# Kernel tuning notes

Hardware: AMD Instinct MI355X
Metric: run time of the kernel (lower is better)

The kernel has to match this reference:

```python
import jax, jax.numpy as jnp
import numpy as np
from functools import partial

D_MODEL, D_STATE, D_CONV, EXPAND = 1024, 16, 4, 2
D_INNER = D_MODEL * EXPAND
B_SZ, L = 4, 2048


def setup_inputs() -> dict:
    key = jax.random.key(0)
    ks = jax.random.split(key, 8)
    s = 0.02
    A_init = jnp.log(jnp.arange(1, D_STATE + 1, dtype=jnp.float32))
    return {
        "x": jax.random.normal(ks[0], (B_SZ, L, D_MODEL), jnp.float32),
        "norm_w": jnp.ones((D_MODEL,), jnp.float32),
        "norm_b": jnp.zeros((D_MODEL,), jnp.float32),
        "W_in": jax.random.normal(ks[1], (D_MODEL, 2 * D_INNER), jnp.float32) * s,
        "conv_w": jax.random.normal(ks[2], (D_INNER, 1, D_CONV), jnp.float32) * 0.3,
        "conv_b": jnp.zeros((D_INNER,), jnp.float32),
        "A_log": jnp.broadcast_to(A_init, (D_INNER, D_STATE)).copy(),
        "W_b": jax.random.normal(ks[3], (D_INNER, D_STATE), jnp.float32) * s,
        "W_c": jax.random.normal(ks[4], (D_INNER, D_STATE), jnp.float32) * s,
        "W_delta": jax.random.normal(ks[5], (D_INNER, D_INNER), jnp.float32) * s,
        "b_delta": jnp.zeros((D_INNER,), jnp.float32),
        "D_param": jnp.ones((D_INNER,), jnp.float32),
        "W_out": jax.random.normal(ks[6], (D_INNER, D_MODEL), jnp.float32) * s,
    }


def _layernorm(x, w, b, eps=1e-5):
    mu = jnp.mean(x, axis=-1, keepdims=True)
    var = jnp.mean(jnp.square(x - mu), axis=-1, keepdims=True)
    return (x - mu) * jax.lax.rsqrt(var + eps) * w + b


def reference(x, norm_w, norm_b, W_in, conv_w, conv_b, A_log, W_b, W_c,
              W_delta, b_delta, D_param, W_out):
    residual = x
    xn = _layernorm(x, norm_w, norm_b)
    xz = jnp.einsum('bld,de->ble', xn, W_in)  # [B, L, 2*D_inner]
    x_path, z = jnp.split(xz, 2, axis=-1)

    # depthwise causal conv1d (torch pads both sides K-1 then slices [:L] == left-pad K-1)
    xc = jnp.moveaxis(x_path, 1, 2)  # [B, D_inner, L]
    xc = jax.lax.conv_general_dilated(
        xc, conv_w, window_strides=(1,), padding=[(D_CONV - 1, 0)],
        dimension_numbers=('NCH', 'OIH', 'NCH'), feature_group_count=D_INNER)
    xc = xc + conv_b[None, :, None]
    x_path = jax.nn.silu(jnp.moveaxis(xc, 2, 1))  # [B, L, D_inner]

    Bm = jnp.einsum('bld,dn->bln', x_path, W_b)   # [B, L, N]
    Cm = jnp.einsum('bld,dn->bln', x_path, W_c)   # [B, L, N]
    delta = jax.nn.softplus(jnp.einsum('bld,de->ble', x_path, W_delta) + b_delta)
    A = -jnp.exp(A_log)  # [D_inner, N]

    def step(h, inp):
        xt, dt, Bt, Ct = inp  # xt,dt: [B,D]; Bt,Ct: [B,N]
        A_bar = jnp.exp(dt[..., None] * A)              # [B, D, N]
        h = A_bar * h + (dt * xt)[..., None] * Bt[:, None, :]
        y = jnp.einsum('bdn,bn->bd', h, Ct) + D_param * xt
        return h, y

    h0 = jnp.zeros((x.shape[0], D_INNER, D_STATE), x_path.dtype)
    xs = (jnp.moveaxis(x_path, 1, 0), jnp.moveaxis(delta, 1, 0),
          jnp.moveaxis(Bm, 1, 0), jnp.moveaxis(Cm, 1, 0))
    _, ys = jax.lax.scan(step, h0, xs)           # ys: [L, B, D_inner]
    y = jnp.moveaxis(ys, 0, 1)                   # [B, L, D_inner]

    return jnp.einsum('bld,de->ble', y * jax.nn.silu(z), W_out) + residual
```

## Files before the change

### kernel.cpp

```cpp
#include <hip/hip_runtime.h>
#include <hip/hip_bf16.h>

#define D_MODEL 1024
#define D_STATE 16
#define D_INNER 2048
#define BSZ     4
#define SEQ     2048
#define NTOK    (BSZ*SEQ)
#define NBIG    2176
#define NCH     16
#define TC      128

typedef __attribute__((ext_vector_type(8))) short short8;
typedef __attribute__((ext_vector_type(4))) float floatx4;

__device__ __forceinline__ ushort bf2us(float f)
{
    union { __hip_bfloat16 h; ushort u; } c;
    c.h = __float2bfloat16(f);
    return c.u;
}
__device__ __forceinline__ float us2f(ushort u)
{
    union { uint u; float f; } c;
    c.u = ((uint)u) << 16;
    return c.f;
}
__device__ __forceinline__ uint pk2(float a, float b)
{
    return (uint)bf2us(a) | ((uint)bf2us(b) << 16);
}
__device__ __forceinline__ float blo(uint u) { return __uint_as_float(u << 16); }
__device__ __forceinline__ float bhi(uint u) { return __uint_as_float(u & 0xffff0000u); }
__device__ __forceinline__ float softplus_f(float v)
{
    return (v > 20.f) ? v : __logf(1.f + __expf(v));
}

__device__ __forceinline__ void load_lds16(const __hip_bfloat16* g, __hip_bfloat16* l)
{
    __builtin_amdgcn_global_load_lds(
        (const __attribute__((address_space(1))) char*)g,
        (__attribute__((address_space(3))) char*)l, 16, 0, 0);
}

__global__ __launch_bounds__(256) void ln_kernel(
    const float* __restrict__ x, const float* __restrict__ w,
    const float* __restrict__ bvec, __hip_bfloat16* __restrict__ out)
{
    int token = blockIdx.x;
    int tid = threadIdx.x;
    const float4 v = ((const float4*)(x + (size_t)token * D_MODEL))[tid];
    float s  = v.x + v.y + v.z + v.w;
    float sq = v.x*v.x + v.y*v.y + v.z*v.z + v.w*v.w;
#pragma unroll
    for (int o = 32; o; o >>= 1) { s += __shfl_down(s, o, 64); sq += __shfl_down(sq, o, 64); }
    __shared__ float red[8];
    int wid = tid >> 6;
    if ((tid & 63) == 0) { red[wid] = s; red[wid + 4] = sq; }
    __syncthreads();
    s  = red[0] + red[1] + red[2] + red[3];
    sq = red[4] + red[5] + red[6] + red[7];
    float mu  = s * (1.f / D_MODEL);
    float var = sq * (1.f / D_MODEL) - mu * mu;
    float rs  = rsqrtf(var + 1e-5f);
    float4 wv = ((const float4*)w)[tid];
    float4 bv = ((const float4*)bvec)[tid];
    union { ushort4 u; __hip_bfloat16 h[4]; } p;
    p.h[0] = __float2bfloat16((v.x - mu) * rs * wv.x + bv.x);
    p.h[1] = __float2bfloat16((v.y - mu) * rs * wv.y + bv.y);
    p.h[2] = __float2bfloat16((v.z - mu) * rs * wv.z + bv.z);
    p.h[3] = __float2bfloat16((v.w - mu) * rs * wv.w + bv.w);
    ((ushort4*)(out + (size_t)token * D_MODEL))[tid] = p.u;
}

__device__ __forceinline__ void tr_body(
    const float* __restrict__ src, __hip_bfloat16* __restrict__ dst,
    int R, int C, int dstStride, int dstRowOff, int bx, int by, int tx, int ty)
{
    __shared__ float tile[32][33];
#pragma unroll
    for (int i = 0; i < 4; ++i) {
        int r = by * 32 + ty + i * 8;
        int c = bx * 32 + tx;
        if (r < R && c < C) tile[ty + i * 8][tx] = src[(size_t)r * C + c];
    }
    __syncthreads();
#pragma unroll
    for (int i = 0; i < 4; ++i) {
        int c = bx * 32 + ty + i * 8;
        int r = by * 32 + tx;
        if (c < C && r < R)
            dst[(size_t)(dstRowOff + c) * dstStride + r] = __float2bfloat16(tile[tx][ty + i * 8]);
    }
}

__global__ __launch_bounds__(256) void transpose_cast(
    const float* __restrict__ src, __hip_bfloat16* __restrict__ dst,
    int R, int C, int dstStride, int dstRowOff)
{
    tr_body(src, dst, R, C, dstStride, dstRowOff,
            blockIdx.x, blockIdx.y, threadIdx.x, threadIdx.y);
}

__global__ __launch_bounds__(256) void prep_w(
    const float* __restrict__ W_in, const float* __restrict__ W_delta,
    const float* __restrict__ W_b, const float* __restrict__ W_c,
    __hip_bfloat16* __restrict__ wT1, __hip_bfloat16* __restrict__ wT2)
{
    int s = blockIdx.x;
    int tx = threadIdx.x, ty = threadIdx.y;
    if (s < 4096) {
        tr_body(W_in, wT1, 1024, 4096, 1024, 0, s & 127, s >> 7, tx, ty);
    } else if (s < 8192) {
        int q = s - 4096;
        tr_body(W_delta, wT2, 2048, 2048, 2048, 0, q & 63, q >> 6, tx, ty);
    } else if (s < 8256) {
        tr_body(W_b, wT2, 2048, 16, 2048, 2048, 0, s - 8192, tx, ty);
    } else if (s < 8320) {
        tr_body(W_c, wT2, 2048, 16, 2048, 2064, 0, s - 8256, tx, ty);
    } else {
        int i = (s - 8320) * 256 + ty * 32 + tx;
        uint4 z = {0, 0, 0, 0};
        ((uint4*)(wT2 + (size_t)2080 * 2048))[i] = z;
    }
}

template <int MODE>
__device__ __forceinline__ void gemm_body(
    const __hip_bfloat16* __restrict__ A, const __hip_bfloat16* __restrict__ BT,
    int M, int N, int K,
    float* __restrict__ outF,
    __hip_bfloat16* __restrict__ outB1, __hip_bfloat16* __restrict__ outB2,
    const float* __restrict__ extra)
{
    __shared__ __align__(16) __hip_bfloat16 As[128 * 64];
    __shared__ __align__(16) __hip_bfloat16 Bs[128 * 64];
    int tid = threadIdx.x;
    int m0 = blockIdx.x * 128;
    int n0 = blockIdx.y * 128;
    int wv = tid >> 6, lane = tid & 63;
    int wm = (wv >> 1) * 64, wn = (wv & 1) * 64;
    int lr = lane & 15, lq = lane >> 4;

    int srow = wv * 8 + (lane >> 3);
    int scg  = (lane & 7) ^ (lane >> 3);
    const __hip_bfloat16* Ag = A  + (size_t)(m0 + srow) * K + scg * 8;
    const __hip_bfloat16* Bg = BT + (size_t)(n0 + srow) * K + scg * 8;
    __hip_bfloat16* AsW = As + (wv * 8) * 64;
    __hip_bfloat16* BsW = Bs + (wv * 8) * 64;

    int swz = lq ^ (lr & 7);

    floatx4 acc[4][4] = {};

    for (int k0 = 0; k0 < K; k0 += 64) {
        __syncthreads();
#pragma unroll
        for (int i = 0; i < 4; ++i) {
            load_lds16(Ag + (size_t)(i * 32) * K + k0, AsW + i * 32 * 64);
            load_lds16(Bg + (size_t)(i * 32) * K + k0, BsW + i * 32 * 64);
        }
        __syncthreads();
#pragma unroll
        for (int kk = 0; kk < 2; ++kk) {
            int cofs = (swz ^ (kk << 2)) * 8;
            short8 af[4], bf[4];
#pragma unroll
            for (int mi = 0; mi < 4; ++mi)
                af[mi] = *(const short8*)(As + (wm + mi * 16 + lr) * 64 + cofs);
#pragma unroll
            for (int ni = 0; ni < 4; ++ni)
                bf[ni] = *(const short8*)(Bs + (wn + ni * 16 + lr) * 64 + cofs);
#pragma unroll
            for (int mi = 0; mi < 4; ++mi)
#pragma unroll
                for (int ni = 0; ni < 4; ++ni)
                    acc[mi][ni] = __builtin_amdgcn_mfma_f32_16x16x32_bf16(af[mi], bf[ni], acc[mi][ni], 0, 0, 0);
        }
    }

#pragma unroll
    for (int mi = 0; mi < 4; ++mi)
#pragma unroll
        for (int ni = 0; ni < 4; ++ni)
#pragma unroll
            for (int r = 0; r < 4; ++r) {
                int rg = m0 + wm + mi * 16 + lq * 4 + r;
                int cg = n0 + wn + ni * 16 + lr;
                float v = acc[mi][ni][r];
                if (MODE == 1) {
                    if (cg < D_INNER) {
                        outB1[(size_t)rg * D_INNER + cg] = __float2bfloat16(v);
                    } else {
                        float sv = v / (1.f + __expf(-v));
                        outB2[(size_t)rg * D_INNER + (cg - D_INNER)] = __float2bfloat16(sv);
                    }
                } else if (MODE == 2) {
                    if (cg < D_INNER) {
                        outB1[(size_t)rg * D_INNER + cg] = __float2bfloat16(softplus_f(v + extra[cg]));
                    } else if (cg < D_INNER + 32) {
                        outB2[(size_t)rg * 32 + (cg - D_INNER)] = __float2bfloat16(v);
                    }
                } else {
                    outF[(size_t)rg * D_MODEL + cg] = v + extra[(size_t)rg * D_MODEL + cg];
                }
            }
}

__global__ __launch_bounds__(256) void gemm_xz(
    const __hip_bfloat16* __restrict__ A, const __hip_bfloat16* __restrict__ BT,
    int M, int N, int K, float* __restrict__ outF,
    __hip_bfloat16* __restrict__ o1, __hip_bfloat16* __restrict__ o2,
    const float* __restrict__ extra)
{ gemm_body<1>(A, BT, M, N, K, outF, o1, o2, extra); }

__global__ __launch_bounds__(256) void gemm_dbc(
    const __hip_bfloat16* __restrict__ A, const __hip_bfloat16* __restrict__ BT,
    int M, int N, int K, float* __restrict__ outF,
    __hip_bfloat16* __restrict__ o1, __hip_bfloat16* __restrict__ o2,
    const float* __restrict__ extra)
{ gemm_body<2>(A, BT, M, N, K, outF, o1, o2, extra); }

__global__ __launch_bounds__(256) void gemm_out(
    const __hip_bfloat16* __restrict__ A, const __hip_bfloat16* __restrict__ BT,
    int M, int N, int K, float* __restrict__ outF,
    __hip_bfloat16* __restrict__ o1, __hip_bfloat16* __restrict__ o2,
    const float* __restrict__ extra)
{ gemm_body<3>(A, BT, M, N, K, outF, o1, o2, extra); }

__global__ __launch_bounds__(256) void conv_silu(
    const __hip_bfloat16* __restrict__ xin, const float* __restrict__ cw,
    const float* __restrict__ cb, __hip_bfloat16* __restrict__ xp)
{
    int gid = blockIdx.x * 256 + threadIdx.x;
    int d = gid & (D_INNER - 1);
    int rest = gid >> 11;
    int b = rest & 3;
    int ch = rest >> 2;
    int t0 = ch * 64;
    float w0 = cw[d * 4 + 0], w1 = cw[d * 4 + 1], w2 = cw[d * 4 + 2], w3 = cw[d * 4 + 3];
    float bias = cb[d];
    const __hip_bfloat16* base = xin + (size_t)b * SEQ * D_INNER + d;
    __hip_bfloat16* ob = xp + (size_t)b * SEQ * D_INNER + d;
    float xm3 = (t0 >= 3) ? __bfloat162float(base[(size_t)(t0 - 3) * D_INNER]) : 0.f;
    float xm2 = (t0 >= 2) ? __bfloat162float(base[(size_t)(t0 - 2) * D_INNER]) : 0.f;
    float xm1 = (t0 >= 1) ? __bfloat162float(base[(size_t)(t0 - 1) * D_INNER]) : 0.f;
#pragma unroll 4
    for (int t = t0; t < t0 + 64; ++t) {
        float xcur = __bfloat162float(base[(size_t)t * D_INNER]);
        float v = bias + w0 * xm3 + w1 * xm2 + w2 * xm1 + w3 * xcur;
        float sv = v / (1.f + __expf(-v));
        ob[(size_t)t * D_INNER] = __float2bfloat16(sv);
        xm3 = xm2; xm2 = xm1; xm1 = xcur;
    }
}


#define LOAD_A16() \
    const float4* Ar = (const float4*)(A_log + (size_t)d * D_STATE); \
    float4 aA = Ar[0], aB = Ar[1], aC = Ar[2], aD = Ar[3]; \
    float A0 = -__expf(aA.x), A1 = -__expf(aA.y), A2 = -__expf(aA.z), A3 = -__expf(aA.w); \
    float A4 = -__expf(aB.x), A5 = -__expf(aB.y), A6 = -__expf(aB.z), A7 = -__expf(aB.w); \
    float A8 = -__expf(aC.x), A9 = -__expf(aC.y), A10 = -__expf(aC.z), A11 = -__expf(aC.w); \
    float A12 = -__expf(aD.x), A13 = -__expf(aD.y), A14 = -__expf(aD.z), A15 = -__expf(aD.w)

#define UNPACK16(P, r0, r1) \
    float P##0 = blo(r0.x), P##1 = bhi(r0.x), P##2 = blo(r0.y), P##3 = bhi(r0.y); \
    float P##4 = blo(r0.z), P##5 = bhi(r0.z), P##6 = blo(r0.w), P##7 = bhi(r0.w); \
    float P##8 = blo(r1.x), P##9 = bhi(r1.x), P##10 = blo(r1.y), P##11 = bhi(r1.y); \
    float P##12 = blo(r1.z), P##13 = bhi(r1.z), P##14 = blo(r1.w), P##15 = bhi(r1.w)

#define SCAN_STEP_B() do { \
    float dtx = dt * xt; \
    h0  = __expf(dt * A0)  * h0  + dtx * B0; \
    h1  = __expf(dt * A1)  * h1  + dtx * B1; \
    h2  = __expf(dt * A2)  * h2  + dtx * B2; \
    h3  = __expf(dt * A3)  * h3  + dtx * B3; \
    h4  = __expf(dt * A4)  * h4  + dtx * B4; \
    h5  = __expf(dt * A5)  * h5  + dtx * B5; \
    h6  = __expf(dt * A6)  * h6  + dtx * B6; \
    h7  = __expf(dt * A7)  * h7  + dtx * B7; \
    h8  = __expf(dt * A8)  * h8  + dtx * B8; \
    h9  = __expf(dt * A9)  * h9  + dtx * B9; \
    h10 = __expf(dt * A10) * h10 + dtx * B10; \
    h11 = __expf(dt * A11) * h11 + dtx * B11; \
    h12 = __expf(dt * A12) * h12 + dtx * B12; \
    h13 = __expf(dt * A13) * h13 + dtx * B13; \
    h14 = __expf(dt * A14) * h14 + dtx * B14; \
    h15 = __expf(dt * A15) * h15 + dtx * B15; \
} while (0)

__global__ __launch_bounds__(256) void scan_p1(
    const ushort* __restrict__ dtb, const ushort* __restrict__ xpb,
    const ushort* __restrict__ BC, const float* __restrict__ A_log,
    ushort* __restrict__ hloc, ushort* __restrict__ prod)
{
    int gid = blockIdx.x * 256 + threadIdx.x;
    int d  = gid & (D_INNER - 1);
    int ch = (gid >> 11) & (NCH - 1);
    int b  = gid >> 15;
    LOAD_A16();
    float h0 = 0.f, h1 = 0.f, h2 = 0.f, h3 = 0.f, h4 = 0.f, h5 = 0.f, h6 = 0.f, h7 = 0.f;
    float h8 = 0.f, h9 = 0.f, h10 = 0.f, h11 = 0.f, h12 = 0.f, h13 = 0.f, h14 = 0.f, h15 = 0.f;
    float dtsum = 0.f;
    size_t mBase = (size_t)b * SEQ + (size_t)ch * TC;
    const ushort* dtp = dtb + mBase * D_INNER + d;
    const ushort* xpp = xpb + mBase * D_INNER + d;
    const uint4*  bcp = (const uint4*)(BC + mBase * 32);
    float dt = us2f(dtp[0]);
    float xt = us2f(xpp[0]);
    uint4 r0 = bcp[0], r1 = bcp[1];
    for (int t = 0; t < TC - 1; ++t) {
        float dt_n = us2f(dtp[(size_t)(t + 1) * D_INNER]);
        float xt_n = us2f(xpp[(size_t)(t + 1) * D_INNER]);
        uint4 r0_n = bcp[(t + 1) * 4 + 0];
        uint4 r1_n = bcp[(t + 1) * 4 + 1];
        {
            UNPACK16(B, r0, r1);
            dtsum += dt;
            SCAN_STEP_B();
        }
        dt = dt_n; xt = xt_n; r0 = r0_n; r1 = r1_n;
    }
    {
        UNPACK16(B, r0, r1);
        dtsum += dt;
        SCAN_STEP_B();
    }
    size_t idx = ((size_t)(b * NCH + ch) * D_INNER + d) * D_STATE;
    uint4 ho, h2v, po, p2v;
    ho.x  = pk2(h0, h1);   ho.y  = pk2(h2, h3);
    ho.z  = pk2(h4, h5);   ho.w  = pk2(h6, h7);
    h2v.x = pk2(h8, h9);   h2v.y = pk2(h10, h11);
    h2v.z = pk2(h12, h13); h2v.w = pk2(h14, h15);
    po.x  = pk2(__expf(dtsum * A0),  __expf(dtsum * A1));
    po.y  = pk2(__expf(dtsum * A2),  __expf(dtsum * A3));
    po.z  = pk2(__expf(dtsum * A4),  __expf(dtsum * A5));
    po.w  = pk2(__expf(dtsum * A6),  __expf(dtsum * A7));
    p2v.x = pk2(__expf(dtsum * A8),  __expf(dtsum * A9));
    p2v.y = pk2(__expf(dtsum * A10), __expf(dtsum * A11));
    p2v.z = pk2(__expf(dtsum * A12), __expf(dtsum * A13));
    p2v.w = pk2(__expf(dtsum * A14), __expf(dtsum * A15));
    ((uint4*)(hloc + idx))[0] = ho; ((uint4*)(hloc + idx))[1] = h2v;
    ((uint4*)(prod + idx))[0] = po; ((uint4*)(prod + idx))[1] = p2v;
}

__global__ __launch_bounds__(256) void scan_p2(
    const ushort* __restrict__ dtb, const ushort* __restrict__ xpb,
    const ushort* __restrict__ BC, const float* __restrict__ A_log,
    const float* __restrict__ D_param, const ushort* __restrict__ hloc,
    const ushort* __restrict__ prod, ushort* __restrict__ zio)
{
    int gid = blockIdx.x * 256 + threadIdx.x;
    int d  = gid & (D_INNER - 1);
    int ch = (gid >> 11) & (NCH - 1);
    int b  = gid >> 15;
    LOAD_A16();
    float Dp = D_param[d];
    float h0 = 0.f, h1 = 0.f, h2 = 0.f, h3 = 0.f, h4 = 0.f, h5 = 0.f, h6 = 0.f, h7 = 0.f;
    float h8 = 0.f, h9 = 0.f, h10 = 0.f, h11 = 0.f, h12 = 0.f, h13 = 0.f, h14 = 0.f, h15 = 0.f;
    for (int j = 0; j < ch; ++j) {
        size_t jdx = ((size_t)(b * NCH + j) * D_INNER + d) * D_STATE;
        uint4 a0 = ((const uint4*)(hloc + jdx))[0];
        uint4 a1 = ((const uint4*)(hloc + jdx))[1];
        uint4 q0 = ((const uint4*)(prod + jdx))[0];
        uint4 q1 = ((const uint4*)(prod + jdx))[1];
        h0  = blo(a0.x) + blo(q0.x) * h0;   h1  = bhi(a0.x) + bhi(q0.x) * h1;
        h2  = blo(a0.y) + blo(q0.y) * h2;   h3  = bhi(a0.y) + bhi(q0.y) * h3;
        h4  = blo(a0.z) + blo(q0.z) * h4;   h5  = bhi(a0.z) + bhi(q0.z) * h5;
        h6  = blo(a0.w) + blo(q0.w) * h6;   h7  = bhi(a0.w) + bhi(q0.w) * h7;
        h8  = blo(a1.x) + blo(q1.x) * h8;   h9  = bhi(a1.x) + bhi(q1.x) * h9;
        h10 = blo(a1.y) + blo(q1.y) * h10;  h11 = bhi(a1.y) + bhi(q1.y) * h11;
        h12 = blo(a1.z) + blo(q1.z) * h12;  h13 = bhi(a1.z) + bhi(q1.z) * h13;
        h14 = blo(a1.w) + blo(q1.w) * h14;  h15 = bhi(a1.w) + bhi(q1.w) * h15;
    }
    size_t mBase = (size_t)b * SEQ + (size_t)ch * TC;
    const ushort* dtp = dtb + mBase * D_INNER + d;
    const ushort* xpp = xpb + mBase * D_INNER + d;
    const uint4*  bcp = (const uint4*)(BC + mBase * 32);
    ushort* zp = zio + mBase * D_INNER + d;
    float dt = us2f(dtp[0]);
    float xt = us2f(xpp[0]);
    uint4 r0 = bcp[0], r1 = bcp[1], r2 = bcp[2], r3 = bcp[3];
    for (int t = 0; t < TC; ++t) {
        float dt_n = 0.f, xt_n = 0.f;
        uint4 r0_n = {0,0,0,0}, r1_n = {0,0,0,0}, r2_n = {0,0,0,0}, r3_n = {0,0,0,0};
        if (t < TC - 1) {
            dt_n = us2f(dtp[(size_t)(t + 1) * D_INNER]);
            xt_n = us2f(xpp[(size_t)(t + 1) * D_INNER]);
            r0_n = bcp[(t + 1) * 4 + 0];
            r1_n = bcp[(t + 1) * 4 + 1];
            r2_n = bcp[(t + 1) * 4 + 2];
            r3_n = bcp[(t + 1) * 4 + 3];
        }
        {
            UNPACK16(B, r0, r1);
            UNPACK16(C, r2, r3);
            float dtx = dt * xt;
            float y = Dp * xt;
            h0  = __expf(dt * A0)  * h0  + dtx * B0;   y += h0  * C0;
            h1  = __expf(dt * A1)  * h1  + dtx * B1;   y += h1  * C1;
            h2  = __expf(dt * A2)  * h2  + dtx * B2;   y += h2  * C2;
            h3  = __expf(dt * A3)  * h3  + dtx * B3;   y += h3  * C3;
            h4  = __expf(dt * A4)  * h4  + dtx * B4;   y += h4  * C4;
            h5  = __expf(dt * A5)  * h5  + dtx * B5;   y += h5  * C5;
            h6  = __expf(dt * A6)  * h6  + dtx * B6;   y += h6  * C6;
            h7  = __expf(dt * A7)  * h7  + dtx * B7;   y += h7  * C7;
            h8  = __expf(dt * A8)  * h8  + dtx * B8;   y += h8  * C8;
            h9  = __expf(dt * A9)  * h9  + dtx * B9;   y += h9  * C9;
            h10 = __expf(dt * A10) * h10 + dtx * B10;  y += h10 * C10;
            h11 = __expf(dt * A11) * h11 + dtx * B11;  y += h11 * C11;
            h12 = __expf(dt * A12) * h12 + dtx * B12;  y += h12 * C12;
            h13 = __expf(dt * A13) * h13 + dtx * B13;  y += h13 * C13;
            h14 = __expf(dt * A14) * h14 + dtx * B14;  y += h14 * C14;
            h15 = __expf(dt * A15) * h15 + dtx * B15;  y += h15 * C15;
            float z = us2f(zp[(size_t)t * D_INNER]);
            zp[(size_t)t * D_INNER] = bf2us(y * z);
        }
        dt = dt_n; xt = xt_n; r0 = r0_n; r1 = r1_n; r2 = r2_n; r3 = r3_n;
    }
}

extern "C" void kernel_launch(void* const* d_in, const int* in_sizes, int n_in,
                              void* d_out, int out_size, void* d_ws, size_t ws_size,
                              hipStream_t stream)
{
    const float* x       = (const float*)d_in[0];
    const float* norm_w  = (const float*)d_in[1];
    const float* norm_b  = (const float*)d_in[2];
    const float* W_in    = (const float*)d_in[3];
    const float* conv_w  = (const float*)d_in[4];
    const float* conv_b  = (const float*)d_in[5];
    const float* A_log   = (const float*)d_in[6];
    const float* W_b     = (const float*)d_in[7];
    const float* W_c     = (const float*)d_in[8];
    const float* W_delta = (const float*)d_in[9];
    const float* b_delta = (const float*)d_in[10];
    const float* D_param = (const float*)d_in[11];
    const float* W_out   = (const float*)d_in[12];
    float* out = (float*)d_out;

    char* ws = (char*)d_ws;
    char* R1 = ws;
    char* R2 = R1 + (size_t)33554432;
    char* R3 = R2 + (size_t)33554432;
    char* R4 = R3 + (size_t)33554432;
    char* R5 = R4 + (size_t)8912896;

    __hip_bfloat16* xnb  = (__hip_bfloat16*)R1;
    __hip_bfloat16* wT1  = (__hip_bfloat16*)(R1 + 16777216);
    __hip_bfloat16* xp   = (__hip_bfloat16*)R1;
    __hip_bfloat16* xraw = (__hip_bfloat16*)R2;
    __hip_bfloat16* dtb  = (__hip_bfloat16*)R2;
    __hip_bfloat16* wT3  = (__hip_bfloat16*)R2;
    __hip_bfloat16* zio  = (__hip_bfloat16*)R3;
    __hip_bfloat16* wT2  = (__hip_bfloat16*)R4;
    ushort*         hloc = (ushort*)R4;
    ushort*         prodb= (ushort*)(R4 + 4194304);
    __hip_bfloat16* BCb  = (__hip_bfloat16*)R5;

    ln_kernel<<<NTOK, 256, 0, stream>>>(x, norm_w, norm_b, xnb);

    prep_w<<<8416, dim3(32, 8), 0, stream>>>(W_in, W_delta, W_b, W_c, wT1, wT2);

    gemm_xz<<<dim3(NTOK / 128, 4096 / 128), 256, 0, stream>>>(
        xnb, wT1, NTOK, 4096, 1024, nullptr, xraw, zio, nullptr);

    conv_silu<<<1024, 256, 0, stream>>>(xraw, conv_w, conv_b, xp);

    gemm_dbc<<<dim3(NTOK / 128, NBIG / 128), 256, 0, stream>>>(
        xp, wT2, NTOK, NBIG, 2048, nullptr, dtb, BCb, b_delta);

    scan_p1<<<512, 256, 0, stream>>>((const ushort*)dtb, (const ushort*)xp,
                                     (const ushort*)BCb, A_log, hloc, prodb);
    scan_p2<<<512, 256, 0, stream>>>((const ushort*)dtb, (const ushort*)xp,
                                     (const ushort*)BCb, A_log, D_param,
                                     hloc, prodb, (ushort*)zio);

    transpose_cast<<<dim3(32, 64), dim3(32, 8), 0, stream>>>(W_out, wT3, 2048, 1024, 2048, 0);

    gemm_out<<<dim3(NTOK / 128, D_MODEL / 128), 256, 0, stream>>>(
        zio, wT3, NTOK, D_MODEL, 2048, out, nullptr, nullptr, x);

    (void)in_sizes; (void)n_in; (void)out_size; (void)ws_size;
}
```

Baseline: 568.8 us.

## Use 256x256 double-buffered GEMM for in-proj and delta, split-K B/C GEMM

Replaces the 128x128 GEMMs for the input projection and the delta projection with a new 256x256-tile, 512-thread kernel. It double-buffers LDS, prefetches the next K tile during MFMA phases, and raises wave priority around the MFMA blocks. The small B/C projection is moved out of the padded delta GEMM into a dedicated split-K kernel that writes fp32 partials, followed by a reduction kernel that converts them to bf16. The aim is more data reuse per tile and no wasted padded columns, at the cost of 128KB of LDS per block, lower occupancy, and an extra launch plus a scratch buffer for the partials.

```diff
diff --git a/kernel.cpp b/kernel.cpp
--- a/kernel.cpp
+++ b/kernel.cpp
@@ -7,7 +7,6 @@
 #define BSZ     4
 #define SEQ     2048
 #define NTOK    (BSZ*SEQ)
-#define NBIG    2176
 #define NCH     16
 #define TC      128
 
@@ -126,6 +125,124 @@
     }
 }
 
+
+#define G256_STG_A(kt_, pb_) do { \
+    const __hip_bfloat16* s_ = Ag + (size_t)(kt_) * 64; \
+    __hip_bfloat16* d_ = &As[pb_][wv * 512]; \
+    load_lds16(s_,                   d_); \
+    load_lds16(s_ + (size_t)64 * K,  d_ + 4096); \
+    load_lds16(s_ + (size_t)128 * K, d_ + 8192); \
+    load_lds16(s_ + (size_t)192 * K, d_ + 12288); \
+} while (0)
+
+#define G256_STG_B(kt_, pb_) do { \
+    const __hip_bfloat16* s_ = Bg + (size_t)(kt_) * 64; \
+    __hip_bfloat16* d_ = &Bs[pb_][wv * 512]; \
+    load_lds16(s_,                   d_); \
+    load_lds16(s_ + (size_t)64 * K,  d_ + 4096); \
+    load_lds16(s_ + (size_t)128 * K, d_ + 8192); \
+    load_lds16(s_ + (size_t)192 * K, d_ + 12288); \
+} while (0)
+
+#define G256_PHASE(mih_, nih_, ...) do { \
+    short8 af_[4][2], bf_[2][2]; \
+    _Pragma("unroll") \
+    for (int mi4 = 0; mi4 < 4; ++mi4) \
+      _Pragma("unroll") \
+      for (int kk = 0; kk < 2; ++kk) \
+        af_[mi4][kk] = *(const short8*)&As[p][((wm * 128 + ((mih_)*4 + mi4) * 16 + lr) << 6) \
+                                             + ((lq ^ (kk << 2) ^ (lr & 7)) << 3)]; \
+    _Pragma("unroll") \
+    for (int ni2 = 0; ni2 < 2; ++ni2) \
+      _Pragma("unroll") \
+      for (int kk = 0; kk < 2; ++kk) \
+        bf_[ni2][kk] = *(const short8*)&Bs[p][((wn * 64 + ((nih_)*2 + ni2) * 16 + lr) << 6) \
+                                             + ((lq ^ (kk << 2) ^ (lr & 7)) << 3)]; \
+    __VA_ARGS__; \
+    __builtin_amdgcn_s_barrier(); \
+    __builtin_amdgcn_s_setprio(1); \
+    _Pragma("unroll") \
+    for (int kk = 0; kk < 2; ++kk) \
+      _Pragma("unroll") \
+      for (int mi4 = 0; mi4 < 4; ++mi4) \
+        _Pragma("unroll") \
+        for (int ni2 = 0; ni2 < 2; ++ni2) \
+          acc[(mih_)*4 + mi4][(nih_)*2 + ni2] = __builtin_amdgcn_mfma_f32_16x16x32_bf16( \
+              af_[mi4][kk], bf_[ni2][kk], acc[(mih_)*4 + mi4][(nih_)*2 + ni2], 0, 0, 0); \
+    __builtin_amdgcn_s_setprio(0); \
+    __builtin_amdgcn_s_barrier(); \
+} while (0)
+
+template <int MODE, int K>
+__device__ __forceinline__ void gemm256_body(
+    const __hip_bfloat16* __restrict__ A, const __hip_bfloat16* __restrict__ BT,
+    __hip_bfloat16* __restrict__ out1, __hip_bfloat16* __restrict__ out2,
+    const float* __restrict__ extra)
+{
+    __shared__ __align__(16) __hip_bfloat16 As[2][256 * 64];
+    __shared__ __align__(16) __hip_bfloat16 Bs[2][256 * 64];
+    const int tid = threadIdx.x;
+    const int wv = tid >> 6, lane = tid & 63;
+    const int wm = wv >> 2, wn = wv & 3;
+    const int lr = lane & 15, lq = lane >> 4;
+    const int m0 = blockIdx.x * 256, n0 = blockIdx.y * 256;
+    const int srow8 = lane >> 3;
+    const int scg = (lane & 7) ^ srow8;
+    const __hip_bfloat16* Ag = A  + (size_t)(m0 + wv * 8 + srow8) * K + scg * 8;
+    const __hip_bfloat16* Bg = BT + (size_t)(n0 + wv * 8 + srow8) * K + scg * 8;
+
+    floatx4 acc[8][4] = {};
+    constexpr int NT = K / 64;
+
+    G256_STG_A(0, 0);
+    G256_STG_B(0, 0);
+    asm volatile("s_waitcnt vmcnt(0)" ::: "memory");
+    __builtin_amdgcn_s_barrier();
+
+#pragma unroll 2
+    for (int kt = 0; kt < NT; ++kt) {
+        const int p = kt & 1;
+        const bool pf = (kt + 1 < NT);
+        G256_PHASE(0, 0, if (pf) G256_STG_A(kt + 1, p ^ 1));
+        G256_PHASE(0, 1, if (pf) G256_STG_B(kt + 1, p ^ 1));
+        G256_PHASE(1, 0, (void)0);
+        G256_PHASE(1, 1, (void)0);
+        asm volatile("s_waitcnt vmcnt(0)" ::: "memory");
+        __builtin_amdgcn_s_barrier();
+    }
+
+#pragma unroll
+    for (int mi = 0; mi < 8; ++mi)
+#pragma unroll
+        for (int ni = 0; ni < 4; ++ni)
+#pragma unroll
+            for (int r = 0; r < 4; ++r) {
+                int rg = m0 + wm * 128 + mi * 16 + lq * 4 + r;
+                int cg = n0 + wn * 64 + ni * 16 + lr;
+                float v = acc[mi][ni][r];
+                if (MODE == 1) {
+                    if (cg < D_INNER) {
+                        out1[(size_t)rg * D_INNER + cg] = __float2bfloat16(v);
+                    } else {
+                        float sv = v / (1.f + __expf(-v));
+                        out2[(size_t)rg * D_INNER + (cg - D_INNER)] = __float2bfloat16(sv);
+                    }
+                } else {
+                    out1[(size_t)rg * D_INNER + cg] = __float2bfloat16(softplus_f(v + extra[cg]));
+                }
+            }
+}
+
+__global__ __launch_bounds__(512, 2) void gemm256_xz(
+    const __hip_bfloat16* __restrict__ A, const __hip_bfloat16* __restrict__ BT,
+    __hip_bfloat16* __restrict__ o1, __hip_bfloat16* __restrict__ o2)
+{ gemm256_body<1, 1024>(A, BT, o1, o2, nullptr); }
+
+__global__ __launch_bounds__(512, 2) void gemm256_dt(
+    const __hip_bfloat16* __restrict__ A, const __hip_bfloat16* __restrict__ BT,
+    __hip_bfloat16* __restrict__ o1, const float* __restrict__ extra)
+{ gemm256_body<2, 2048>(A, BT, o1, nullptr, extra); }
+
 template <int MODE>
 __device__ __forceinline__ void gemm_body(
     const __hip_bfloat16* __restrict__ A, const __hip_bfloat16* __restrict__ BT,
@@ -189,38 +306,10 @@
                 int rg = m0 + wm + mi * 16 + lq * 4 + r;
                 int cg = n0 + wn + ni * 16 + lr;
                 float v = acc[mi][ni][r];
-                if (MODE == 1) {
-                    if (cg < D_INNER) {
-                        outB1[(size_t)rg * D_INNER + cg] = __float2bfloat16(v);
-                    } else {
-                        float sv = v / (1.f + __expf(-v));
-                        outB2[(size_t)rg * D_INNER + (cg - D_INNER)] = __float2bfloat16(sv);
-                    }
-                } else if (MODE == 2) {
-                    if (cg < D_INNER) {
-                        outB1[(size_t)rg * D_INNER + cg] = __float2bfloat16(softplus_f(v + extra[cg]));
-                    } else if (cg < D_INNER + 32) {
-                        outB2[(size_t)rg * 32 + (cg - D_INNER)] = __float2bfloat16(v);
-                    }
-                } else {
-                    outF[(size_t)rg * D_MODEL + cg] = v + extra[(size_t)rg * D_MODEL + cg];
-                }
+                (void)outB1; (void)outB2;
+                outF[(size_t)rg * D_MODEL + cg] = v + extra[(size_t)rg * D_MODEL + cg];
             }
 }
-
-__global__ __launch_bounds__(256) void gemm_xz(
-    const __hip_bfloat16* __restrict__ A, const __hip_bfloat16* __restrict__ BT,
-    int M, int N, int K, float* __restrict__ outF,
-    __hip_bfloat16* __restrict__ o1, __hip_bfloat16* __restrict__ o2,
-    const float* __restrict__ extra)
-{ gemm_body<1>(A, BT, M, N, K, outF, o1, o2, extra); }
-
-__global__ __launch_bounds__(256) void gemm_dbc(
-    const __hip_bfloat16* __restrict__ A, const __hip_bfloat16* __restrict__ BT,
-    int M, int N, int K, float* __restrict__ outF,
-    __hip_bfloat16* __restrict__ o1, __hip_bfloat16* __restrict__ o2,
-    const float* __restrict__ extra)
-{ gemm_body<2>(A, BT, M, N, K, outF, o1, o2, extra); }
 
 __global__ __launch_bounds__(256) void gemm_out(
     const __hip_bfloat16* __restrict__ A, const __hip_bfloat16* __restrict__ BT,
@@ -228,6 +317,64 @@
     __hip_bfloat16* __restrict__ o1, __hip_bfloat16* __restrict__ o2,
     const float* __restrict__ extra)
 { gemm_body<3>(A, BT, M, N, K, outF, o1, o2, extra); }
+
+__global__ __launch_bounds__(256) void gemm_bc(
+    const __hip_bfloat16* __restrict__ xp, const __hip_bfloat16* __restrict__ wbc,
+    float* __restrict__ part)
+{
+    __shared__ __align__(16) __hip_bfloat16 As[128 * 64];
+    __shared__ __align__(16) __hip_bfloat16 Bs[32 * 64];
+    int tid = threadIdx.x, wv = tid >> 6, lane = tid & 63;
+    int lr = lane & 15, lq = lane >> 4;
+    int m0 = blockIdx.x * 128;
+    int k0s = blockIdx.y * 512;
+    int srow8 = lane >> 3, scg = (lane & 7) ^ srow8;
+    const __hip_bfloat16* Ag = xp  + (size_t)(m0 + wv * 8 + srow8) * 2048 + k0s + scg * 8;
+    const __hip_bfloat16* Bg = wbc + (size_t)(wv * 8 + srow8) * 2048 + k0s + scg * 8;
+    floatx4 acc[2][2] = {};
+    for (int k0 = 0; k0 < 512; k0 += 64) {
+        __syncthreads();
+#pragma unroll
+        for (int i = 0; i < 4; ++i)
+            load_lds16(Ag + (size_t)(i * 32) * 2048 + k0, As + (wv * 8 + i * 32) * 64);
+        if (wv < 4) load_lds16(Bg + k0, Bs + wv * 8 * 64);
+        __syncthreads();
+#pragma unroll
+        for (int kk = 0; kk < 2; ++kk) {
+            int cofs = (lq ^ (kk << 2) ^ (lr & 7)) * 8;
+            short8 a0 = *(const short8*)(As + (wv * 32 + lr) * 64 + cofs);
+            short8 a1 = *(const short8*)(As + (wv * 32 + 16 + lr) * 64 + cofs);
+            short8 b0 = *(const short8*)(Bs + (lr) * 64 + cofs);
+            short8 b1 = *(const short8*)(Bs + (16 + lr) * 64 + cofs);
+            acc[0][0] = __builtin_amdgcn_mfma_f32_16x16x32_bf16(a0, b0, acc[0][0], 0, 0, 0);
+            acc[0][1] = __builtin_amdgcn_mfma_f32_16x16x32_bf16(a0, b1, acc[0][1], 0, 0, 0);
+            acc[1][0] = __builtin_amdgcn_mfma_f32_16x16x32_bf16(a1, b0, acc[1][0], 0, 0, 0);
+            acc[1][1] = __builtin_amdgcn_mfma_f32_16x16x32_bf16(a1, b1, acc[1][1], 0, 0, 0);
+        }
+    }
+    float* pb = part + (size_t)blockIdx.y * (NTOK * 32);
+#pragma unroll
+    for (int mi = 0; mi < 2; ++mi)
+#pragma unroll
+        for (int ni = 0; ni < 2; ++ni)
+#pragma unroll
+            for (int r = 0; r < 4; ++r)
+                pb[(size_t)(m0 + wv * 32 + mi * 16 + lq * 4 + r) * 32 + ni * 16 + lr] = acc[mi][ni][r];
+}
+
+__global__ __launch_bounds__(256) void cvt_bc(
+    const float* __restrict__ part, ushort* __restrict__ out)
+{
+    int i = blockIdx.x * 256 + threadIdx.x;
+    const float4* p = (const float4*)part;
+    float4 a = p[i], b = p[i + 65536], c = p[i + 131072], d = p[i + 196608];
+    ushort4 o;
+    o.x = bf2us(a.x + b.x + c.x + d.x);
+    o.y = bf2us(a.y + b.y + c.y + d.y);
+    o.z = bf2us(a.z + b.z + c.z + d.z);
+    o.w = bf2us(a.w + b.w + c.w + d.w);
+    ((ushort4*)out)[i] = o;
+}
 
 __global__ __launch_bounds__(256) void conv_silu(
     const __hip_bfloat16* __restrict__ xin, const float* __restrict__ cw,
@@ -452,6 +599,7 @@
     __hip_bfloat16* wT1  = (__hip_bfloat16*)(R1 + 16777216);
     __hip_bfloat16* xp   = (__hip_bfloat16*)R1;
     __hip_bfloat16* xraw = (__hip_bfloat16*)R2;
+    float*          BCf  = (float*)R2;
     __hip_bfloat16* dtb  = (__hip_bfloat16*)R2;
     __hip_bfloat16* wT3  = (__hip_bfloat16*)R2;
     __hip_bfloat16* zio  = (__hip_bfloat16*)R3;
@@ -464,13 +612,14 @@
 
     prep_w<<<8416, dim3(32, 8), 0, stream>>>(W_in, W_delta, W_b, W_c, wT1, wT2);
 
-    gemm_xz<<<dim3(NTOK / 128, 4096 / 128), 256, 0, stream>>>(
-        xnb, wT1, NTOK, 4096, 1024, nullptr, xraw, zio, nullptr);
+    gemm256_xz<<<dim3(32, 16), 512, 0, stream>>>(xnb, wT1, xraw, zio);
 
     conv_silu<<<1024, 256, 0, stream>>>(xraw, conv_w, conv_b, xp);
 
-    gemm_dbc<<<dim3(NTOK / 128, NBIG / 128), 256, 0, stream>>>(
-        xp, wT2, NTOK, NBIG, 2048, nullptr, dtb, BCb, b_delta);
+    gemm_bc<<<dim3(64, 4), 256, 0, stream>>>(xp, wT2 + (size_t)2048 * 2048, BCf);
+    cvt_bc<<<256, 256, 0, stream>>>(BCf, (ushort*)BCb);
+
+    gemm256_dt<<<dim3(32, 8), 512, 0, stream>>>(xp, wT2, dtb, b_delta);
 
     scan_p1<<<512, 256, 0, stream>>>((const ushort*)dtb, (const ushort*)xp,
                                      (const ushort*)BCb, A_log, hloc, prodb);
```

New measurement: 559.1 us. No clear change (-1.7%).
